# Performance work log

Hardware: AMD Instinct MI355X
Metric: run time of the kernel (lower is better)

Reference implementation:

```python
import jax, jax.numpy as jnp
import numpy as np

HIDDEN = 768  # hidden_dim of the embedding matrix
VOCAB = 30522


def setup_inputs() -> dict:
    key = jax.random.key(0)
    k1, k2, k3, k4, k5, k6 = jax.random.split(key, 6)
    core = jax.random.normal(k1, (40, 256, 256), dtype=jnp.float32)
    f0 = jax.random.normal(k2, (40, 40), dtype=jnp.float32)
    f1 = jax.random.normal(k3, (768, 256), dtype=jnp.float32)
    f2 = jax.random.normal(k4, (768, 256), dtype=jnp.float32)
    ids = jax.random.randint(k5, (8192,), 0, VOCAB, dtype=jnp.int32)
    x = jax.random.normal(k6, (8192, 768), dtype=jnp.float32)  # unused by forward, kept for signature parity
    return {"x": x, "ids": ids, "core": core, "f0": f0, "f1": f1, "f2": f2}


def reference(x, ids, core, f0, f1, f2):
    # tucker_to_tensor: core x_0 f0 x_1 f1 x_2 f2 -> (40, 768, 768)
    res = jnp.einsum('abc,ia,jb,kc->ijk', core, f0, f1, f2)
    # flatten to padded embedding table (30720, 768) and gather requested rows
    table = res.reshape(-1, HIDDEN)
    return table[ids, :]
```

## Files before the change

kernel.cpp:

```cpp
#include <hip/hip_runtime.h>


#define A_DIM 40
#define BC 65536
#define C_DIM 256
#define HID 768

typedef __attribute__((ext_vector_type(8))) short short8;
typedef __attribute__((ext_vector_type(4))) float floatx4;

#define AS1 __attribute__((address_space(1)))
#define AS3 __attribute__((address_space(3)))

__device__ __forceinline__ void gl2lds16(const unsigned short* g, unsigned short* l) {
    __builtin_amdgcn_global_load_lds((const AS1 unsigned int*)g, (AS3 unsigned int*)l,
                                     16, 0, 0);
}

__device__ __forceinline__ unsigned short f2bf(float f) {
    unsigned int u = __builtin_bit_cast(unsigned int, f);
    u += 0x7FFFu + ((u >> 16) & 1u);
    return (unsigned short)(u >> 16);
}

__global__ __launch_bounds__(256) void k0_cvt(const float* __restrict__ f1,
                                              const float* __restrict__ f2,
                                              unsigned short* __restrict__ f1b,
                                              unsigned short* __restrict__ f2b) {
    const int idx = blockIdx.x * 256 + threadIdx.x;
    const float* src;
    unsigned short* dst;
    int off;
    if (idx < 49152) { src = f1; dst = f1b; off = idx; }
    else             { src = f2; dst = f2b; off = idx - 49152; }
    const float4 v = *(const float4*)&src[off * 4];
    const unsigned int lo = (unsigned int)f2bf(v.x) | ((unsigned int)f2bf(v.y) << 16);
    const unsigned int hi = (unsigned int)f2bf(v.z) | ((unsigned int)f2bf(v.w) << 16);
    *(uint2*)&dst[off * 4] = make_uint2(lo, hi);
}

__global__ __launch_bounds__(256) void k1_mode0(const float* __restrict__ core,
                                                const float* __restrict__ f0,
                                                unsigned short* __restrict__ A1) {
    __shared__ float f0s[A_DIM * A_DIM];
    for (int e = threadIdx.x; e < A_DIM * A_DIM; e += 256) f0s[e] = f0[e];
    __syncthreads();
    const int bc = blockIdx.x * 256 + threadIdx.x;
    float acc[A_DIM];
#pragma unroll
    for (int i = 0; i < A_DIM; ++i) acc[i] = 0.f;
    for (int a = 0; a < A_DIM; ++a) {
        const float cv = core[a * BC + bc];
#pragma unroll
        for (int i = 0; i < A_DIM; ++i) acc[i] += f0s[i * A_DIM + a] * cv;
    }
#pragma unroll
    for (int i = 0; i < A_DIM; ++i) A1[i * BC + bc] = f2bf(acc[i]);
}

__global__ __launch_bounds__(256) void k1_transpose(const unsigned short* __restrict__ A1,
                                                    unsigned short* __restrict__ A1t) {
    const int i  = blockIdx.z;
    const int b0 = blockIdx.x * 64;
    const int c0 = blockIdx.y * 64;
    const unsigned short* __restrict__ src = A1 + i * BC;
    unsigned short* __restrict__ dst = A1t + i * BC;
    __shared__ unsigned short tile[64 * 66];
    const int t = threadIdx.x;
#pragma unroll
    for (int h = 0; h < 2; ++h) {
        const int s = t + h * 256;
        const int r = s >> 3, cs = (s & 7) * 8;
        short8 v = *(const short8*)&src[(b0 + r) * 256 + c0 + cs];
#pragma unroll
        for (int u = 0; u < 8; ++u) tile[r * 66 + cs + u] = ((unsigned short*)&v)[u];
    }
    __syncthreads();
#pragma unroll
    for (int h = 0; h < 2; ++h) {
        const int s = t + h * 256;
        const int c = s >> 3, bs = (s & 7) * 8;
        short8 o;
#pragma unroll
        for (int u = 0; u < 8; ++u) ((unsigned short*)&o)[u] = tile[(bs + u) * 66 + c];
        *(short8*)&dst[(c0 + c) * 256 + b0 + bs] = o;
    }
}

__global__ __launch_bounds__(256) void k2_gemm(const unsigned short* __restrict__ f1b,
                                               const unsigned short* __restrict__ A1t,
                                               unsigned short* __restrict__ A2) {
    const int i  = blockIdx.z;
    const int j0 = blockIdx.x * 128;
    const int c0 = blockIdx.y * 128;
    const unsigned short* __restrict__ Bsrc = A1t + i * BC;

    __shared__ unsigned short As[128 * 32];
    __shared__ unsigned short Bs[128 * 32];

    const int tid = threadIdx.x;
    const int lane = tid & 63, wave = tid >> 6;
    const int wm = (wave >> 1) * 64, wn = (wave & 1) * 64;
    const int l16 = lane & 15, q = lane >> 4;

    const int r_lo = tid >> 2,         o_lo = (tid & 3) * 8;
    const int r_hi = (tid + 256) >> 2, o_hi = (tid & 3) * 8;
    unsigned short* AsW0 = &As[wave * 512];
    unsigned short* AsW1 = &As[2048 + wave * 512];
    unsigned short* BsW0 = &Bs[wave * 512];
    unsigned short* BsW1 = &Bs[2048 + wave * 512];

    floatx4 acc[4][4];
#pragma unroll
    for (int p = 0; p < 4; ++p)
#pragma unroll
        for (int r = 0; r < 4; ++r) acc[p][r] = (floatx4)0.f;

    for (int kk = 0; kk < C_DIM; kk += 32) {
        gl2lds16(&f1b[(j0 + r_lo) * 256 + kk + o_lo], AsW0);
        gl2lds16(&f1b[(j0 + r_hi) * 256 + kk + o_hi], AsW1);
        gl2lds16(&Bsrc[(c0 + r_lo) * 256 + kk + o_lo], BsW0);
        gl2lds16(&Bsrc[(c0 + r_hi) * 256 + kk + o_hi], BsW1);
        __syncthreads();
        short8 af[4], bf[4];
#pragma unroll
        for (int p = 0; p < 4; ++p) af[p] = *(const short8*)&As[(wm + p * 16 + l16) * 32 + q * 8];
#pragma unroll
        for (int r = 0; r < 4; ++r) bf[r] = *(const short8*)&Bs[(wn + r * 16 + l16) * 32 + q * 8];
#pragma unroll
        for (int p = 0; p < 4; ++p)
#pragma unroll
            for (int r = 0; r < 4; ++r)
                acc[p][r] = __builtin_amdgcn_mfma_f32_16x16x32_bf16(af[p], bf[r], acc[p][r], 0, 0, 0);
        __syncthreads();
    }
    unsigned short* __restrict__ Cout = A2 + (size_t)i * HID * C_DIM;
#pragma unroll
    for (int p = 0; p < 4; ++p)
#pragma unroll
        for (int r = 0; r < 4; ++r)
#pragma unroll
            for (int rr = 0; rr < 4; ++rr) {
                const int row = j0 + wm + p * 16 + q * 4 + rr;
                const int col = c0 + wn + r * 16 + l16;
                Cout[row * 256 + col] = f2bf(acc[p][r][rr]);
            }
}

__global__ __launch_bounds__(256) void k3_gemm(const unsigned short* __restrict__ A2,
                                               const unsigned short* __restrict__ f2b,
                                               const int* __restrict__ ids,
                                               float* __restrict__ out) {
    const int n0 = blockIdx.x * 128;
    const int k0 = blockIdx.y * 128;

    __shared__ int ids_s[128];
    __shared__ unsigned short As[128 * 32];
    __shared__ unsigned short Bs[128 * 32];

    const int tid = threadIdx.x;
    if (tid < 128) ids_s[tid] = ids[n0 + tid];
    __syncthreads();

    const int lane = tid & 63, wave = tid >> 6;
    const int wm = (wave >> 1) * 64, wn = (wave & 1) * 64;
    const int l16 = lane & 15, q = lane >> 4;

    const int r_lo = tid >> 2,         o_lo = (tid & 3) * 8;
    const int r_hi = (tid + 256) >> 2, o_hi = (tid & 3) * 8;
    const size_t ga = (size_t)ids_s[r_lo] * 256;
    const size_t gb = (size_t)ids_s[r_hi] * 256;
    unsigned short* AsW0 = &As[wave * 512];
    unsigned short* AsW1 = &As[2048 + wave * 512];
    unsigned short* BsW0 = &Bs[wave * 512];
    unsigned short* BsW1 = &Bs[2048 + wave * 512];

    floatx4 acc[4][4];
#pragma unroll
    for (int p = 0; p < 4; ++p)
#pragma unroll
        for (int r = 0; r < 4; ++r) acc[p][r] = (floatx4)0.f;

    for (int kk = 0; kk < C_DIM; kk += 32) {
        gl2lds16(&A2[ga + kk + o_lo], AsW0);
        gl2lds16(&A2[gb + kk + o_hi], AsW1);
        gl2lds16(&f2b[(k0 + r_lo) * 256 + kk + o_lo], BsW0);
        gl2lds16(&f2b[(k0 + r_hi) * 256 + kk + o_hi], BsW1);
        __syncthreads();
        short8 af[4], bf[4];
#pragma unroll
        for (int p = 0; p < 4; ++p) af[p] = *(const short8*)&As[(wm + p * 16 + l16) * 32 + q * 8];
#pragma unroll
        for (int r = 0; r < 4; ++r) bf[r] = *(const short8*)&Bs[(wn + r * 16 + l16) * 32 + q * 8];
#pragma unroll
        for (int p = 0; p < 4; ++p)
#pragma unroll
            for (int r = 0; r < 4; ++r)
                acc[p][r] = __builtin_amdgcn_mfma_f32_16x16x32_bf16(af[p], bf[r], acc[p][r], 0, 0, 0);
        __syncthreads();
    }
#pragma unroll
    for (int p = 0; p < 4; ++p)
#pragma unroll
        for (int r = 0; r < 4; ++r)
#pragma unroll
            for (int rr = 0; rr < 4; ++rr) {
                const int row = n0 + wm + p * 16 + q * 4 + rr;
                const int col = k0 + wn + r * 16 + l16;
                out[(size_t)row * HID + col] = acc[p][r][rr];
            }
}

extern "C" void kernel_launch(void* const* d_in, const int* in_sizes, int n_in,
                              void* d_out, int out_size, void* d_ws, size_t ws_size,
                              hipStream_t stream) {
    const int*   ids  = (const int*)d_in[1];
    const float* core = (const float*)d_in[2];
    const float* f0   = (const float*)d_in[3];
    const float* f1   = (const float*)d_in[4];
    const float* f2   = (const float*)d_in[5];
    float* out = (float*)d_out;

    char* ws = (char*)d_ws;
    unsigned short* A1  = (unsigned short*)ws;
    unsigned short* A1t = (unsigned short*)(ws + 5242880);
    unsigned short* A2  = (unsigned short*)(ws + 10485760);
    unsigned short* f1b = (unsigned short*)(ws + 26214400);
    unsigned short* f2b = (unsigned short*)(ws + 26607616);

    k0_cvt<<<384, 256, 0, stream>>>(f1, f2, f1b, f2b);
    k1_mode0<<<256, 256, 0, stream>>>(core, f0, A1);
    k1_transpose<<<dim3(4, 4, A_DIM), 256, 0, stream>>>(A1, A1t);
    k2_gemm<<<dim3(6, 2, A_DIM), 256, 0, stream>>>(f1b, A1t, A2);
    k3_gemm<<<dim3(64, 6), 256, 0, stream>>>(A2, f2b, ids, out);
}
```

Measured before the change: 127.5 us.

## Fuse convert with mode-0 contraction, split its output rows, and shrink GEMM tiles

The bf16 conversion kernel and the mode-0 contraction now run as one launch. The contraction is split into four blocks per column chunk, each computing 10 output rows, which gives 1024 blocks instead of 256. Both MFMA GEMMs drop from 128x128 to 64x64 tiles, giving four times as many workgroups to fill the GPU's many compute units. In exchange, smaller tiles mean less reuse per load, and the mode-0 blocks now re-read the core tensor four times.

```diff
diff --git a/kernel.cpp b/kernel.cpp
--- a/kernel.cpp
+++ b/kernel.cpp
@@ -23,39 +23,42 @@
     return (unsigned short)(u >> 16);
 }
 
-__global__ __launch_bounds__(256) void k0_cvt(const float* __restrict__ f1,
-                                              const float* __restrict__ f2,
-                                              unsigned short* __restrict__ f1b,
-                                              unsigned short* __restrict__ f2b) {
-    const int idx = blockIdx.x * 256 + threadIdx.x;
-    const float* src;
-    unsigned short* dst;
-    int off;
-    if (idx < 49152) { src = f1; dst = f1b; off = idx; }
-    else             { src = f2; dst = f2b; off = idx - 49152; }
-    const float4 v = *(const float4*)&src[off * 4];
-    const unsigned int lo = (unsigned int)f2bf(v.x) | ((unsigned int)f2bf(v.y) << 16);
-    const unsigned int hi = (unsigned int)f2bf(v.z) | ((unsigned int)f2bf(v.w) << 16);
-    *(uint2*)&dst[off * 4] = make_uint2(lo, hi);
-}
-
-__global__ __launch_bounds__(256) void k1_mode0(const float* __restrict__ core,
-                                                const float* __restrict__ f0,
-                                                unsigned short* __restrict__ A1) {
-    __shared__ float f0s[A_DIM * A_DIM];
-    for (int e = threadIdx.x; e < A_DIM * A_DIM; e += 256) f0s[e] = f0[e];
-    __syncthreads();
-    const int bc = blockIdx.x * 256 + threadIdx.x;
-    float acc[A_DIM];
-#pragma unroll
-    for (int i = 0; i < A_DIM; ++i) acc[i] = 0.f;
-    for (int a = 0; a < A_DIM; ++a) {
-        const float cv = core[a * BC + bc];
-#pragma unroll
-        for (int i = 0; i < A_DIM; ++i) acc[i] += f0s[i * A_DIM + a] * cv;
-    }
-#pragma unroll
-    for (int i = 0; i < A_DIM; ++i) A1[i * BC + bc] = f2bf(acc[i]);
+__global__ __launch_bounds__(256) void k01_cvt_mode0(const float* __restrict__ core,
+                                                     const float* __restrict__ f0,
+                                                     const float* __restrict__ f1,
+                                                     const float* __restrict__ f2,
+                                                     unsigned short* __restrict__ A1,
+                                                     unsigned short* __restrict__ f1b,
+                                                     unsigned short* __restrict__ f2b) {
+    const int bid = blockIdx.x;
+    if (bid < 1024) {
+        __shared__ float f0s[A_DIM * A_DIM];
+        const int i0 = (bid >> 8) * 10;
+        for (int e = threadIdx.x; e < A_DIM * A_DIM; e += 256) f0s[e] = f0[e];
+        __syncthreads();
+        const int bc = (bid & 255) * 256 + threadIdx.x;
+        float acc[10];
+#pragma unroll
+        for (int ii = 0; ii < 10; ++ii) acc[ii] = 0.f;
+        for (int a = 0; a < A_DIM; ++a) {
+            const float cv = core[a * BC + bc];
+#pragma unroll
+            for (int ii = 0; ii < 10; ++ii) acc[ii] += f0s[(i0 + ii) * A_DIM + a] * cv;
+        }
+#pragma unroll
+        for (int ii = 0; ii < 10; ++ii) A1[(i0 + ii) * BC + bc] = f2bf(acc[ii]);
+    } else {
+        const int idx = (bid - 1024) * 256 + threadIdx.x;
+        const float* src;
+        unsigned short* dst;
+        int off;
+        if (idx < 49152) { src = f1; dst = f1b; off = idx; }
+        else             { src = f2; dst = f2b; off = idx - 49152; }
+        const float4 v = *(const float4*)&src[off * 4];
+        const unsigned int lo = (unsigned int)f2bf(v.x) | ((unsigned int)f2bf(v.y) << 16);
+        const unsigned int hi = (unsigned int)f2bf(v.z) | ((unsigned int)f2bf(v.w) << 16);
+        *(uint2*)&dst[off * 4] = make_uint2(lo, hi);
+    }
 }
 
 __global__ __launch_bounds__(256) void k1_transpose(const unsigned short* __restrict__ A1,
@@ -91,54 +94,49 @@
                                                const unsigned short* __restrict__ A1t,
                                                unsigned short* __restrict__ A2) {
     const int i  = blockIdx.z;
-    const int j0 = blockIdx.x * 128;
-    const int c0 = blockIdx.y * 128;
+    const int j0 = blockIdx.x * 64;
+    const int c0 = blockIdx.y * 64;
     const unsigned short* __restrict__ Bsrc = A1t + i * BC;
 
-    __shared__ unsigned short As[128 * 32];
-    __shared__ unsigned short Bs[128 * 32];
+    __shared__ unsigned short As[64 * 32];
+    __shared__ unsigned short Bs[64 * 32];
 
     const int tid = threadIdx.x;
     const int lane = tid & 63, wave = tid >> 6;
-    const int wm = (wave >> 1) * 64, wn = (wave & 1) * 64;
+    const int wm = (wave >> 1) * 32, wn = (wave & 1) * 32;
     const int l16 = lane & 15, q = lane >> 4;
 
-    const int r_lo = tid >> 2,         o_lo = (tid & 3) * 8;
-    const int r_hi = (tid + 256) >> 2, o_hi = (tid & 3) * 8;
-    unsigned short* AsW0 = &As[wave * 512];
-    unsigned short* AsW1 = &As[2048 + wave * 512];
-    unsigned short* BsW0 = &Bs[wave * 512];
-    unsigned short* BsW1 = &Bs[2048 + wave * 512];
-
-    floatx4 acc[4][4];
-#pragma unroll
-    for (int p = 0; p < 4; ++p)
-#pragma unroll
-        for (int r = 0; r < 4; ++r) acc[p][r] = (floatx4)0.f;
+    const int r0 = tid >> 2, o0 = (tid & 3) * 8;
+    unsigned short* AsW = &As[wave * 512];
+    unsigned short* BsW = &Bs[wave * 512];
+
+    floatx4 acc[2][2];
+#pragma unroll
+    for (int p = 0; p < 2; ++p)
+#pragma unroll
+        for (int r = 0; r < 2; ++r) acc[p][r] = (floatx4)0.f;
 
     for (int kk = 0; kk < C_DIM; kk += 32) {
-        gl2lds16(&f1b[(j0 + r_lo) * 256 + kk + o_lo], AsW0);
-        gl2lds16(&f1b[(j0 + r_hi) * 256 + kk + o_hi], AsW1);
-        gl2lds16(&Bsrc[(c0 + r_lo) * 256 + kk + o_lo], BsW0);
-        gl2lds16(&Bsrc[(c0 + r_hi) * 256 + kk + o_hi], BsW1);
-        __syncthreads();
-        short8 af[4], bf[4];
-#pragma unroll
-        for (int p = 0; p < 4; ++p) af[p] = *(const short8*)&As[(wm + p * 16 + l16) * 32 + q * 8];
-#pragma unroll
-        for (int r = 0; r < 4; ++r) bf[r] = *(const short8*)&Bs[(wn + r * 16 + l16) * 32 + q * 8];
-#pragma unroll
-        for (int p = 0; p < 4; ++p)
-#pragma unroll
-            for (int r = 0; r < 4; ++r)
+        gl2lds16(&f1b[(j0 + r0) * 256 + kk + o0], AsW);
+        gl2lds16(&Bsrc[(c0 + r0) * 256 + kk + o0], BsW);
+        __syncthreads();
+        short8 af[2], bf[2];
+#pragma unroll
+        for (int p = 0; p < 2; ++p) af[p] = *(const short8*)&As[(wm + p * 16 + l16) * 32 + q * 8];
+#pragma unroll
+        for (int r = 0; r < 2; ++r) bf[r] = *(const short8*)&Bs[(wn + r * 16 + l16) * 32 + q * 8];
+#pragma unroll
+        for (int p = 0; p < 2; ++p)
+#pragma unroll
+            for (int r = 0; r < 2; ++r)
                 acc[p][r] = __builtin_amdgcn_mfma_f32_16x16x32_bf16(af[p], bf[r], acc[p][r], 0, 0, 0);
         __syncthreads();
     }
     unsigned short* __restrict__ Cout = A2 + (size_t)i * HID * C_DIM;
 #pragma unroll
-    for (int p = 0; p < 4; ++p)
-#pragma unroll
-        for (int r = 0; r < 4; ++r)
+    for (int p = 0; p < 2; ++p)
+#pragma unroll
+        for (int r = 0; r < 2; ++r)
 #pragma unroll
             for (int rr = 0; rr < 4; ++rr) {
                 const int row = j0 + wm + p * 16 + q * 4 + rr;
@@ -151,58 +149,52 @@
                                                const unsigned short* __restrict__ f2b,
                                                const int* __restrict__ ids,
                                                float* __restrict__ out) {
-    const int n0 = blockIdx.x * 128;
-    const int k0 = blockIdx.y * 128;
-
-    __shared__ int ids_s[128];
-    __shared__ unsigned short As[128 * 32];
-    __shared__ unsigned short Bs[128 * 32];
+    const int n0 = blockIdx.x * 64;
+    const int k0 = blockIdx.y * 64;
+
+    __shared__ int ids_s[64];
+    __shared__ unsigned short As[64 * 32];
+    __shared__ unsigned short Bs[64 * 32];
 
     const int tid = threadIdx.x;
-    if (tid < 128) ids_s[tid] = ids[n0 + tid];
+    if (tid < 64) ids_s[tid] = ids[n0 + tid];
     __syncthreads();
 
     const int lane = tid & 63, wave = tid >> 6;
-    const int wm = (wave >> 1) * 64, wn = (wave & 1) * 64;
+    const int wm = (wave >> 1) * 32, wn = (wave & 1) * 32;
     const int l16 = lane & 15, q = lane >> 4;
 
-    const int r_lo = tid >> 2,         o_lo = (tid & 3) * 8;
-    const int r_hi = (tid + 256) >> 2, o_hi = (tid & 3) * 8;
-    const size_t ga = (size_t)ids_s[r_lo] * 256;
-    const size_t gb = (size_t)ids_s[r_hi] * 256;
-    unsigned short* AsW0 = &As[wave * 512];
-    unsigned short* AsW1 = &As[2048 + wave * 512];
-    unsigned short* BsW0 = &Bs[wave * 512];
-    unsigned short* BsW1 = &Bs[2048 + wave * 512];
-
-    floatx4 acc[4][4];
-#pragma unroll
-    for (int p = 0; p < 4; ++p)
-#pragma unroll
-        for (int r = 0; r < 4; ++r) acc[p][r] = (floatx4)0.f;
+    const int r0 = tid >> 2, o0 = (tid & 3) * 8;
+    const size_t ga = (size_t)ids_s[r0] * 256;
+    unsigned short* AsW = &As[wave * 512];
+    unsigned short* BsW = &Bs[wave * 512];
+
+    floatx4 acc[2][2];
+#pragma unroll
+    for (int p = 0; p < 2; ++p)
+#pragma unroll
+        for (int r = 0; r < 2; ++r) acc[p][r] = (floatx4)0.f;
 
     for (int kk = 0; kk < C_DIM; kk += 32) {
-        gl2lds16(&A2[ga + kk + o_lo], AsW0);
-        gl2lds16(&A2[gb + kk + o_hi], AsW1);
-        gl2lds16(&f2b[(k0 + r_lo) * 256 + kk + o_lo], BsW0);
-        gl2lds16(&f2b[(k0 + r_hi) * 256 + kk + o_hi], BsW1);
-        __syncthreads();
-        short8 af[4], bf[4];
-#pragma unroll
-        for (int p = 0; p < 4; ++p) af[p] = *(const short8*)&As[(wm + p * 16 + l16) * 32 + q * 8];
-#pragma unroll
-        for (int r = 0; r < 4; ++r) bf[r] = *(const short8*)&Bs[(wn + r * 16 + l16) * 32 + q * 8];
-#pragma unroll
-        for (int p = 0; p < 4; ++p)
-#pragma unroll
-            for (int r = 0; r < 4; ++r)
+        gl2lds16(&A2[ga + kk + o0], AsW);
+        gl2lds16(&f2b[(k0 + r0) * 256 + kk + o0], BsW);
+        __syncthreads();
+        short8 af[2], bf[2];
+#pragma unroll
+        for (int p = 0; p < 2; ++p) af[p] = *(const short8*)&As[(wm + p * 16 + l16) * 32 + q * 8];
+#pragma unroll
+        for (int r = 0; r < 2; ++r) bf[r] = *(const short8*)&Bs[(wn + r * 16 + l16) * 32 + q * 8];
+#pragma unroll
+        for (int p = 0; p < 2; ++p)
+#pragma unroll
+            for (int r = 0; r < 2; ++r)
                 acc[p][r] = __builtin_amdgcn_mfma_f32_16x16x32_bf16(af[p], bf[r], acc[p][r], 0, 0, 0);
         __syncthreads();
     }
 #pragma unroll
-    for (int p = 0; p < 4; ++p)
-#pragma unroll
-        for (int r = 0; r < 4; ++r)
+    for (int p = 0; p < 2; ++p)
+#pragma unroll
+        for (int r = 0; r < 2; ++r)
 #pragma unroll
             for (int rr = 0; rr < 4; ++rr) {
                 const int row = n0 + wm + p * 16 + q * 4 + rr;
@@ -228,9 +220,8 @@
     unsigned short* f1b = (unsigned short*)(ws + 26214400);
     unsigned short* f2b = (unsigned short*)(ws + 26607616);
 
-    k0_cvt<<<384, 256, 0, stream>>>(f1, f2, f1b, f2b);
-    k1_mode0<<<256, 256, 0, stream>>>(core, f0, A1);
+    k01_cvt_mode0<<<1408, 256, 0, stream>>>(core, f0, f1, f2, A1, f1b, f2b);
     k1_transpose<<<dim3(4, 4, A_DIM), 256, 0, stream>>>(A1, A1t);
-    k2_gemm<<<dim3(6, 2, A_DIM), 256, 0, stream>>>(f1b, A1t, A2);
-    k3_gemm<<<dim3(64, 6), 256, 0, stream>>>(A2, f2b, ids, out);
-}
+    k2_gemm<<<dim3(12, 4, A_DIM), 256, 0, stream>>>(f1b, A1t, A2);
+    k3_gemm<<<dim3(128, 12), 256, 0, stream>>>(A2, f2b, ids, out);
+}
```

New measurement: 118.3 us. -7.2%, faster.
